# Kernel optimization log

Hardware: AMD Instinct MI355X
Metric: run time of the kernel (lower is better)

The kernel has to match this reference:

```python
import jax, jax.numpy as jnp
import numpy as np

WS = 8          # window size -> N = 64
SHIFT = 4       # shift size for shifted windows
FEAT = 32       # feature map H = W at stage 3
C = 512         # channels (SwinV2-B stage 3)
HEADS = 16
B_IMG = 128     # images -> 128 * (32/8)^2 = 2048 windows


def _rel_coords_table():
    # log-spaced continuous relative coords table, SwinV2 style: [(2W-1)^2, 2]
    r = np.arange(-(WS - 1), WS, dtype=np.float32)
    t = np.stack(np.meshgrid(r, r, indexing='ij'), axis=-1)  # [15,15,2]
    t = t / (WS - 1) * 8.0
    t = np.sign(t) * np.log2(np.abs(t) + 1.0) / np.log2(8.0)
    return t.reshape(-1, 2)


def _rel_pos_index():
    c = np.stack(np.meshgrid(np.arange(WS), np.arange(WS), indexing='ij'))  # [2,8,8]
    cf = c.reshape(2, -1)
    rel = (cf[:, :, None] - cf[:, None, :]).transpose(1, 2, 0)  # [64,64,2]
    rel[:, :, 0] += WS - 1
    rel[:, :, 1] += WS - 1
    rel[:, :, 0] *= 2 * WS - 1
    return rel.sum(-1).astype(np.int32)  # [64,64]


def _shift_mask():
    # standard SwinV2 shifted-window attention mask: [nW, N, N] in {0, -100}
    img = np.zeros((FEAT, FEAT), dtype=np.float32)
    cnt = 0
    for hs in (slice(0, -WS), slice(-WS, -SHIFT), slice(-SHIFT, None)):
        for ws in (slice(0, -WS), slice(-WS, -SHIFT), slice(-SHIFT, None)):
            img[hs, ws] = cnt
            cnt += 1
    win = img.reshape(FEAT // WS, WS, FEAT // WS, WS).transpose(0, 2, 1, 3)
    win = win.reshape(-1, WS * WS)  # [nW, 64]
    diff = win[:, None, :] - win[:, :, None]
    return np.where(diff != 0, -100.0, 0.0).astype(np.float32)


def setup_inputs() -> dict:
    key = jax.random.key(0)
    ks = jax.random.split(key, 10)
    nW = (FEAT // WS) ** 2  # 16 windows per image
    Bw = B_IMG * nW         # 2048
    N = WS * WS
    s = 0.02
    return {
        'x': jax.random.normal(ks[0], (Bw, N, C), jnp.float32),
        'mask': jnp.asarray(_shift_mask()),
        'qkv_w': jax.random.normal(ks[1], (3 * C, C), jnp.float32) * s,
        'q_bias': jnp.zeros((C,), jnp.float32),
        'v_bias': jnp.zeros((C,), jnp.float32),
        'logit_scale': jnp.full((HEADS, 1, 1), np.log(10.0), jnp.float32),
        'cpb_w1': jax.random.normal(ks[2], (512, 2), jnp.float32) * s,
        'cpb_b1': jnp.zeros((512,), jnp.float32),
        'cpb_w2': jax.random.normal(ks[3], (HEADS, 512), jnp.float32) * s,
        'proj_w': jax.random.normal(ks[4], (C, C), jnp.float32) * s,
        'proj_b': jnp.zeros((C,), jnp.float32),
        'rel_coords_table': jnp.asarray(_rel_coords_table()),
        'rel_pos_index': jnp.asarray(_rel_pos_index()),
    }


def reference(x, mask, qkv_w, q_bias, v_bias, logit_scale, cpb_w1, cpb_b1,
              cpb_w2, proj_w, proj_b, rel_coords_table, rel_pos_index):
    Bw, N, Cdim = x.shape
    H = logit_scale.shape[0]
    d = Cdim // H
    # qkv projection; k has no bias (SwinV2)
    qkv_bias = jnp.concatenate([q_bias, jnp.zeros_like(q_bias), v_bias])
    qkv = (x @ qkv_w.T + qkv_bias).reshape(Bw, N, 3, H, d).transpose(2, 0, 3, 1, 4)
    q, k, v = qkv[0], qkv[1], qkv[2]  # each [Bw,H,N,d]
    # cosine attention with learned per-head temperature
    qn = q / jnp.maximum(jnp.linalg.norm(q, axis=-1, keepdims=True), 1e-12)
    kn = k / jnp.maximum(jnp.linalg.norm(k, axis=-1, keepdims=True), 1e-12)
    attn = jnp.einsum('bhnd,bhmd->bhnm', qn, kn)
    scale = jnp.exp(jnp.minimum(logit_scale, jnp.log(100.0)))  # [H,1,1]
    attn = attn * scale[None]
    # continuous relative position bias via small MLP over log-spaced coords
    tbl = jax.nn.relu(rel_coords_table @ cpb_w1.T + cpb_b1) @ cpb_w2.T  # [(2W-1)^2,H]
    bias = tbl[rel_pos_index.reshape(-1)].reshape(N, N, H).transpose(2, 0, 1)
    attn = attn + 16.0 * jax.nn.sigmoid(bias)[None]
    # shifted-window mask applied per window group
    nW = mask.shape[0]
    attn = attn.reshape(Bw // nW, nW, H, N, N) + mask[None, :, None]
    attn = jax.nn.softmax(attn.reshape(Bw, H, N, N), axis=-1)
    out = jnp.einsum('bhnm,bhmd->bhnd', attn, v)
    out = out.transpose(0, 2, 1, 3).reshape(Bw, N, Cdim)
    return out @ proj_w.T + proj_b
```

## Files before the change

kernel.cpp:

```cpp
#include <hip/hip_runtime.h>
#include <stdint.h>
#include <stddef.h>


typedef __attribute__((ext_vector_type(8))) short bf16x8;
typedef __attribute__((ext_vector_type(4))) float f32x4;
typedef __attribute__((ext_vector_type(4))) unsigned short us4;
typedef __attribute__((ext_vector_type(8))) unsigned short us8;
typedef unsigned short u16;
typedef unsigned int u32;

#define FENCE() asm volatile("" ::: "memory")
#define WAITV4() asm volatile("s_waitcnt vmcnt(4)" ::: "memory")
#define WAITV3() asm volatile("s_waitcnt vmcnt(3)" ::: "memory")
#define WAITV0() asm volatile("s_waitcnt vmcnt(0)" ::: "memory")
#define WAITL0() asm volatile("s_waitcnt lgkmcnt(0)" ::: "memory")

__device__ __forceinline__ u16 f2bf(float f) {
  union { __bf16 b; u16 u; } cv;
  cv.b = (__bf16)f;
  return cv.u;
}
__device__ __forceinline__ float bf2f(u16 s) {
  return __uint_as_float(((u32)s) << 16);
}
__device__ __forceinline__ void gl_lds16(const void* g, void* l) {
  __builtin_amdgcn_global_load_lds(
      (const __attribute__((address_space(1))) u32*)g,
      (__attribute__((address_space(3))) u32*)l, 16, 0, 0);
}
__device__ __forceinline__ f32x4 mfma16(bf16x8 a, bf16x8 b, f32x4 c) {
  return __builtin_amdgcn_mfma_f32_16x16x32_bf16(a, b, c, 0, 0, 0);
}
__device__ __forceinline__ bf16x8 ldswz(const u16* p, int ks) {
  return *(const bf16x8*)((const u16*)((uintptr_t)p ^ (uintptr_t)(ks << 6)));
}


__global__ void conv_w_kernel(const float* __restrict__ QW, const float* __restrict__ PW,
                              u16* __restrict__ WQB, u16* __restrict__ WPB) {
  int idx = blockIdx.x * 256 + threadIdx.x;
  const int NQ = 1536 * 512 / 4;
  float4 v; u16* dst;
  if (idx < NQ) { v = ((const float4*)QW)[idx]; dst = WQB + (size_t)idx * 4; }
  else { int k = idx - NQ; v = ((const float4*)PW)[k]; dst = WPB + (size_t)k * 4; }
  us4 u; u.x = f2bf(v.x); u.y = f2bf(v.y); u.z = f2bf(v.z); u.w = f2bf(v.w);
  *(us4*)dst = u;
}

__global__ void xconv_kernel(const float* __restrict__ X, u16* __restrict__ XB) {
  size_t idx = (size_t)blockIdx.x * 256 + threadIdx.x;
  float4 a = ((const float4*)X)[idx * 2];
  float4 b = ((const float4*)X)[idx * 2 + 1];
  us8 o;
  o[0] = f2bf(a.x); o[1] = f2bf(a.y); o[2] = f2bf(a.z); o[3] = f2bf(a.w);
  o[4] = f2bf(b.x); o[5] = f2bf(b.y); o[6] = f2bf(b.z); o[7] = f2bf(b.w);
  *(us8*)&XB[idx * 8] = o;
}

__global__ void sig16_kernel(const float* __restrict__ CT, const float* __restrict__ W1,
                             const float* __restrict__ B1, const float* __restrict__ W2,
                             float* __restrict__ SIG) {
  int i = blockIdx.x;
  int tid = threadIdx.x;
  float c0 = CT[i * 2 + 0], c1 = CT[i * 2 + 1];
  float a[16];
  #pragma unroll
  for (int hh = 0; hh < 16; ++hh) a[hh] = 0.f;
  #pragma unroll
  for (int jj = 0; jj < 2; ++jj) {
    int j = tid + jj * 256;
    float h = fmaxf(c0 * W1[j * 2 + 0] + c1 * W1[j * 2 + 1] + B1[j], 0.f);
    #pragma unroll
    for (int hh = 0; hh < 16; ++hh) a[hh] += h * W2[hh * 512 + j];
  }
  __shared__ float red[4][16];
  #pragma unroll
  for (int hh = 0; hh < 16; ++hh) {
    float v = a[hh];
    for (int m = 1; m < 64; m <<= 1) v += __shfl_xor(v, m);
    if ((tid & 63) == 0) red[tid >> 6][hh] = v;
  }
  __syncthreads();
  if (tid < 16) {
    float v = red[0][tid] + red[1][tid] + red[2][tid] + red[3][tid];
    SIG[i * 16 + tid] = 16.f / (1.f + __expf(-v));
  }
}

__global__ void cmb_kernel(const float* __restrict__ SIG, const float* __restrict__ MASK,
                           const int* __restrict__ RPI, float* __restrict__ CMB) {
  int b = blockIdx.x;
  int w = b >> 4, h = b & 15;
  int tid = threadIdx.x;
  const float* mrow = &MASK[(size_t)w * 4096];
  float* crow = &CMB[(size_t)b * 4096];
  #pragma unroll
  for (int it = 0; it < 16; ++it) {
    int nm = it * 256 + tid;
    crow[nm] = SIG[RPI[nm] * 16 + h] + mrow[nm];
  }
}


#define GEMM32_KLOOP()                                                     \
  _Pragma("unroll")                                                        \
  for (int t = 0; t < 16; ++t) {                                           \
    const int Sb = (t % 3) * 12288;                                        \
    _Pragma("unroll")                                                      \
    for (int m = 0; m < 4; ++m)                                            \
      af[m] = *(const bf16x8*)&S[Sb + (wm * 64 + m * 16 + fr) * 32 + fsw]; \
    _Pragma("unroll")                                                      \
    for (int n = 0; n < 2; ++n)                                            \
      bf[n] = *(const bf16x8*)&S[Sb + 4096 + (wn * 64 + n * 16 + fr) * 32 + fsw]; \
    if (t + 2 <= 15) stageB(t + 2);                                        \
    FENCE(); __builtin_amdgcn_s_barrier(); FENCE();                        \
    WAITL0(); __builtin_amdgcn_sched_barrier(0);                           \
    __builtin_amdgcn_s_setprio(1);                                         \
    _Pragma("unroll")                                                      \
    for (int m = 0; m < 4; ++m)                                            \
      _Pragma("unroll")                                                    \
      for (int n = 0; n < 2; ++n)                                          \
        acc[m][n] = mfma16(af[m], bf[n], acc[m][n]);                       \
    __builtin_amdgcn_s_setprio(0);                                         \
    FENCE(); __builtin_amdgcn_s_barrier(); FENCE();                        \
    _Pragma("unroll")                                                      \
    for (int n = 0; n < 2; ++n)                                            \
      bf[n] = *(const bf16x8*)&S[Sb + 4096 + (wn * 64 + (n + 2) * 16 + fr) * 32 + fsw]; \
    if (t + 3 <= 15) stageA(t + 3);                                        \
    if (t <= 12) { WAITV4(); }                                             \
    else if (t == 13) { WAITV3(); }                                        \
    else if (t == 14) { WAITV0(); }                                        \
    FENCE(); __builtin_amdgcn_s_barrier(); FENCE();                        \
    WAITL0(); __builtin_amdgcn_sched_barrier(0);                           \
    __builtin_amdgcn_s_setprio(1);                                         \
    _Pragma("unroll")                                                      \
    for (int m = 0; m < 4; ++m)                                            \
      _Pragma("unroll")                                                    \
      for (int n = 0; n < 2; ++n)                                          \
        acc[m][n + 2] = mfma16(af[m], bf[n], acc[m][n + 2]);               \
    __builtin_amdgcn_s_setprio(0);                                         \
    FENCE(); __builtin_amdgcn_s_barrier(); FENCE();                        \
  }


__global__ __launch_bounds__(512, 4) void qkv_g32(
    const u16* __restrict__ XB, const u16* __restrict__ WB,
    const float* __restrict__ QB, const float* __restrict__ VB,
    u16* __restrict__ QKV) {
  __shared__ u16 S[36864];
  const int tid = threadIdx.x, lane = tid & 63, w = tid >> 6;
  int bid = blockIdx.x;
  int swz = (bid & 7) * 768 + (bid >> 3);
  const int mt = swz / 6, nt = swz - mt * 6;
  const long m0 = (long)mt * 128, n0 = (long)nt * 256;
  const int wm = w >> 2, wn = w & 3;
  const int fr = lane & 15, lg = lane >> 4;
  const int fsw = (lg ^ ((fr >> 1) & 3)) << 3;
  const f32x4 zf = {0.f, 0.f, 0.f, 0.f};

  f32x4 acc[4][4];
  #pragma unroll
  for (int mi = 0; mi < 4; ++mi)
    #pragma unroll
    for (int ni = 0; ni < 4; ++ni) acc[mi][ni] = zf;

  const int arow = tid >> 2;
  const int asc = (tid & 3) ^ ((arow >> 1) & 3);
  const u16* aSrc = &XB[(size_t)(m0 + arow) * 512 + asc * 8];
  const u16* bSrc0 = &WB[(size_t)(n0 + arow) * 512 + asc * 8];
  const u16* bSrc1 = &WB[(size_t)(n0 + 128 + arow) * 512 + asc * 8];

  auto stageA = [&](int kt) {
    gl_lds16(aSrc + kt * 32, &S[(kt % 3) * 12288 + w * 512]);
  };
  auto stageB = [&](int kt) {
    gl_lds16(bSrc0 + kt * 32, &S[(kt % 3) * 12288 + 4096 + w * 512]);
    gl_lds16(bSrc1 + kt * 32, &S[(kt % 3) * 12288 + 8192 + w * 512]);
  };

  bf16x8 af[4], bf[2];

  stageA(0); stageB(0); stageA(1); stageB(1); stageA(2);
  WAITV4();
  FENCE(); __builtin_amdgcn_s_barrier(); FENCE();

  GEMM32_KLOOP()

  u16* eb = &S[w * 4608];
  #pragma unroll
  for (int ni = 0; ni < 4; ++ni) {
    const long c = n0 + wn * 64 + ni * 16 + fr;
    float bias = (c < 512) ? QB[c] : (c < 1024 ? 0.f : VB[c - 1024]);
    #pragma unroll
    for (int mi = 0; mi < 4; ++mi)
      #pragma unroll
      for (int r = 0; r < 4; ++r)
        eb[(mi * 16 + lg * 4 + r) * 72 + ni * 16 + fr] = f2bf(acc[mi][ni][r] + bias);
  }
  WAITL0();
  #pragma unroll
  for (int i = 0; i < 8; ++i) {
    int row = i * 8 + (lane >> 3);
    int c16 = lane & 7;
    us8 v = *(const us8*)&eb[row * 72 + c16 * 8];
    *(us8*)&QKV[(size_t)(m0 + wm * 64 + row) * 1536 + n0 + wn * 64 + c16 * 8] = v;
  }
}


__global__ __launch_bounds__(512, 4) void proj_g32(
    const u16* __restrict__ A, const u16* __restrict__ WB,
    const float* __restrict__ PB, float* __restrict__ OUT) {
  __shared__ u16 S[36864];
  const int tid = threadIdx.x, lane = tid & 63, w = tid >> 6;
  int bid = blockIdx.x;
  int swz = (bid & 7) * 256 + (bid >> 3);
  const int mt = swz >> 1, nt = swz & 1;
  const long m0 = (long)mt * 128, n0 = (long)nt * 256;
  const int wm = w >> 2, wn = w & 3;
  const int fr = lane & 15, lg = lane >> 4;
  const int fsw = (lg ^ ((fr >> 1) & 3)) << 3;
  const f32x4 zf = {0.f, 0.f, 0.f, 0.f};

  f32x4 acc[4][4];
  #pragma unroll
  for (int mi = 0; mi < 4; ++mi)
    #pragma unroll
    for (int ni = 0; ni < 4; ++ni) acc[mi][ni] = zf;

  const int arow = tid >> 2;
  const int asc = (tid & 3) ^ ((arow >> 1) & 3);
  const u16* aSrc = &A[(size_t)(m0 + arow) * 1536 + asc * 8];
  const u16* bSrc0 = &WB[(size_t)(n0 + arow) * 512 + asc * 8];
  const u16* bSrc1 = &WB[(size_t)(n0 + 128 + arow) * 512 + asc * 8];

  auto stageA = [&](int kt) {
    gl_lds16(aSrc + kt * 32, &S[(kt % 3) * 12288 + w * 512]);
  };
  auto stageB = [&](int kt) {
    gl_lds16(bSrc0 + kt * 32, &S[(kt % 3) * 12288 + 4096 + w * 512]);
    gl_lds16(bSrc1 + kt * 32, &S[(kt % 3) * 12288 + 8192 + w * 512]);
  };

  bf16x8 af[4], bf[2];

  stageA(0); stageB(0); stageA(1); stageB(1); stageA(2);
  WAITV4();
  FENCE(); __builtin_amdgcn_s_barrier(); FENCE();

  GEMM32_KLOOP()

  #pragma unroll
  for (int ni = 0; ni < 4; ++ni) {
    const long c = n0 + wn * 64 + ni * 16 + fr;
    float bias = PB[c];
    #pragma unroll
    for (int mi = 0; mi < 4; ++mi)
      #pragma unroll
      for (int r = 0; r < 4; ++r) {
        long row = m0 + wm * 64 + mi * 16 + lg * 4 + r;
        OUT[row * 512 + c] = acc[mi][ni][r] + bias;
      }
  }
}


__global__ __launch_bounds__(256, 2) void qkv_gemm_rs(
    const float* __restrict__ X, const u16* __restrict__ WB,
    const float* __restrict__ QB, const float* __restrict__ VB,
    u16* __restrict__ QKV) {
  __shared__ u16 As[128 * 64];
  __shared__ u16 Bs[128 * 64];
  const int tid = threadIdx.x, lane = tid & 63, w = tid >> 6;
  int bid = blockIdx.x;
  int swz = (bid & 7) * 1536 + (bid >> 3);
  const int mt = swz / 12, nt = swz - mt * 12;
  const long m0 = (long)mt * 128, n0 = (long)nt * 128;
  const int wm = w >> 1, wn = w & 1;
  const f32x4 zf = {0.f, 0.f, 0.f, 0.f};

  f32x4 acc[4][4];
  #pragma unroll
  for (int mi = 0; mi < 4; ++mi)
    #pragma unroll
    for (int ni = 0; ni < 4; ++ni) acc[mi][ni] = zf;

  const int fr = lane & 15;
  const int fsw = ((lane >> 4) ^ (lane & 7)) * 8;
  const u16* Ap = &As[(wm * 64 + fr) * 64 + fsw];
  const u16* Bp = &Bs[(wn * 64 + fr) * 64 + fsw];

  for (int t = 0; t < 8; ++t) {
    float4 av[8];
    #pragma unroll
    for (int i = 0; i < 8; ++i) {
      int ch = tid + (i << 8);
      int row = ch >> 4, kc = ch & 15;
      av[i] = *(const float4*)&X[(m0 + row) * 512 + t * 64 + kc * 4];
    }
    #pragma unroll
    for (int i = 0; i < 4; ++i) {
      int ch = ((w << 2) + i) * 64 + lane;
      int row = ch >> 3, kc = (ch & 7) ^ (row & 7);
      gl_lds16(&WB[(n0 + row) * 512 + t * 64 + kc * 8], &Bs[((w << 2) + i) * 512]);
    }
    #pragma unroll
    for (int i = 0; i < 8; ++i) {
      int ch = tid + (i << 8);
      int row = ch >> 4, kc = ch & 15;
      int kcs = kc ^ ((row & 7) << 1);
      us4 u; u.x = f2bf(av[i].x); u.y = f2bf(av[i].y); u.z = f2bf(av[i].z); u.w = f2bf(av[i].w);
      *(us4*)&As[row * 64 + kcs * 4] = u;
    }
    __syncthreads();
    #pragma unroll
    for (int ks = 0; ks < 2; ++ks) {
      bf16x8 af[4], bfr[4];
      #pragma unroll
      for (int mi = 0; mi < 4; ++mi) af[mi] = ldswz(Ap + mi * 1024, ks);
      #pragma unroll
      for (int ni = 0; ni < 4; ++ni) bfr[ni] = ldswz(Bp + ni * 1024, ks);
      #pragma unroll
      for (int mi = 0; mi < 4; ++mi)
        #pragma unroll
        for (int ni = 0; ni < 4; ++ni)
          acc[mi][ni] = mfma16(af[mi], bfr[ni], acc[mi][ni]);
    }
    __syncthreads();
  }

  #pragma unroll
  for (int ni = 0; ni < 4; ++ni) {
    const long c = n0 + wn * 64 + ni * 16 + (lane & 15);
    float bias = (c < 512) ? QB[c] : (c < 1024 ? 0.f : VB[c - 1024]);
    #pragma unroll
    for (int mi = 0; mi < 4; ++mi)
      #pragma unroll
      for (int r = 0; r < 4; ++r) {
        long row = m0 + wm * 64 + mi * 16 + (lane >> 4) * 4 + r;
        QKV[row * 1536 + c] = f2bf(acc[mi][ni][r] + bias);
      }
  }
}


__global__ __launch_bounds__(256, 3) void attn_wh(
    u16* __restrict__ QKV, const float* __restrict__ CMB, const float* __restrict__ LS) {
  __shared__ u16 smu[26112];
  const int tid = threadIdx.x, lane = tid & 63, w = tid >> 6;
  const int b = blockIdx.x;
  const int win = b >> 2;
  const int h = (b & 3) * 4 + w;
  const int wi = win & 15;
  const size_t base = (size_t)win * 64 * 1536;
  const int fr = lane & 15, lg = lane >> 4;
  u16* ps = &smu[w * 6528];
  u16* vt = ps + 4352;
  const float scale = __expf(fminf(LS[h], 4.6051702f));
  const float* cp = &CMB[((size_t)(wi * 16 + h)) << 12];
  const f32x4 zf = {0.f, 0.f, 0.f, 0.f};

  us8 vrow[4];
  #pragma unroll
  for (int c = 0; c < 4; ++c)
    vrow[c] = *(const us8*)&QKV[base + (size_t)lane * 1536 + 1024 + h * 32 + c * 8];

  f32x4 acc[4][4];
  #pragma unroll
  for (int m = 0; m < 4; ++m)
    #pragma unroll
    for (int n = 0; n < 4; ++n)
      #pragma unroll
      for (int r = 0; r < 4; ++r)
        acc[m][n][r] = cp[(m * 16 + lg * 4 + r) * 64 + n * 16 + fr];

  bf16x8 af[4], bk[4];
  #pragma unroll
  for (int m = 0; m < 4; ++m) {
    us8 qv = *(const us8*)&QKV[base + (size_t)(m * 16 + fr) * 1536 + h * 32 + lg * 8];
    float qf[8]; float ss = 0.f;
    #pragma unroll
    for (int j = 0; j < 8; ++j) { qf[j] = bf2f(qv[j]); ss += qf[j] * qf[j]; }
    ss += __shfl_xor(ss, 16); ss += __shfl_xor(ss, 32);
    float rn = scale / fmaxf(sqrtf(ss), 1e-12f);
    union { us8 u; bf16x8 b; } cv;
    #pragma unroll
    for (int j = 0; j < 8; ++j) cv.u[j] = f2bf(qf[j] * rn);
    af[m] = cv.b;
  }
  #pragma unroll
  for (int m = 0; m < 4; ++m) {
    us8 kv = *(const us8*)&QKV[base + (size_t)(m * 16 + fr) * 1536 + 512 + h * 32 + lg * 8];
    float kf[8]; float ss = 0.f;
    #pragma unroll
    for (int j = 0; j < 8; ++j) { kf[j] = bf2f(kv[j]); ss += kf[j] * kf[j]; }
    ss += __shfl_xor(ss, 16); ss += __shfl_xor(ss, 32);
    float rn = 1.f / fmaxf(sqrtf(ss), 1e-12f);
    union { us8 u; bf16x8 b; } cv;
    #pragma unroll
    for (int j = 0; j < 8; ++j) cv.u[j] = f2bf(kf[j] * rn);
    bk[m] = cv.b;
  }

  #pragma unroll
  for (int m = 0; m < 4; ++m)
    #pragma unroll
    for (int n = 0; n < 4; ++n)
      acc[m][n] = mfma16(af[m], bk[n], acc[m][n]);

  #pragma unroll
  for (int c = 0; c < 4; ++c)
    #pragma unroll
    for (int j = 0; j < 8; ++j)
      vt[(c * 8 + j) * 68 + lane] = vrow[c][j];

  #pragma unroll
  for (int m = 0; m < 4; ++m)
    #pragma unroll
    for (int r = 0; r < 4; ++r) {
      float pv[4];
      float mx = -3.0e38f;
      #pragma unroll
      for (int n = 0; n < 4; ++n) { pv[n] = acc[m][n][r]; mx = fmaxf(mx, pv[n]); }
      mx = fmaxf(mx, __shfl_xor(mx, 1));
      mx = fmaxf(mx, __shfl_xor(mx, 2));
      mx = fmaxf(mx, __shfl_xor(mx, 4));
      mx = fmaxf(mx, __shfl_xor(mx, 8));
      float sum = 0.f;
      #pragma unroll
      for (int n = 0; n < 4; ++n) { pv[n] = __expf(pv[n] - mx); sum += pv[n]; }
      sum += __shfl_xor(sum, 1); sum += __shfl_xor(sum, 2);
      sum += __shfl_xor(sum, 4); sum += __shfl_xor(sum, 8);
      float inv = 1.f / sum;
      #pragma unroll
      for (int n = 0; n < 4; ++n)
        ps[(m * 16 + lg * 4 + r) * 68 + n * 16 + fr] = f2bf(pv[n] * inv);
    }

  WAITL0(); __builtin_amdgcn_sched_barrier(0);

  f32x4 o[4][2];
  #pragma unroll
  for (int m = 0; m < 4; ++m) { o[m][0] = zf; o[m][1] = zf; }
  #pragma unroll
  for (int m = 0; m < 4; ++m)
    #pragma unroll
    for (int ks = 0; ks < 2; ++ks) {
      bf16x8 ap = *(const bf16x8*)&ps[(m * 16 + fr) * 68 + ks * 32 + lg * 8];
      #pragma unroll
      for (int n2 = 0; n2 < 2; ++n2) {
        bf16x8 bv = *(const bf16x8*)&vt[(n2 * 16 + fr) * 68 + ks * 32 + lg * 8];
        o[m][n2] = mfma16(ap, bv, o[m][n2]);
      }
    }

  #pragma unroll
  for (int m = 0; m < 4; ++m)
    #pragma unroll
    for (int n2 = 0; n2 < 2; ++n2)
      #pragma unroll
      for (int r = 0; r < 4; ++r)
        QKV[base + (size_t)(m * 16 + lg * 4 + r) * 1536 + h * 32 + n2 * 16 + fr] =
            f2bf(o[m][n2][r]);
}


extern "C" void kernel_launch(void* const* d_in, const int* in_sizes, int n_in,
                              void* d_out, int out_size, void* d_ws, size_t ws_size,
                              hipStream_t stream) {
  const float* X    = (const float*)d_in[0];
  const float* MASK = (const float*)d_in[1];
  const float* QW   = (const float*)d_in[2];
  const float* QB   = (const float*)d_in[3];
  const float* VB   = (const float*)d_in[4];
  const float* LS   = (const float*)d_in[5];
  const float* CW1  = (const float*)d_in[6];
  const float* CB1  = (const float*)d_in[7];
  const float* CW2  = (const float*)d_in[8];
  const float* PW   = (const float*)d_in[9];
  const float* PB   = (const float*)d_in[10];
  const float* CT   = (const float*)d_in[11];
  const int*   RPI  = (const int*)d_in[12];
  float* OUT = (float*)d_out;

  char* ws = (char*)d_ws;
  const bool big = ws_size >= 543178752ull;
  u16* QKV = (u16*)ws;
  u16* XB  = (u16*)(ws + 402653184ull);
  size_t off = big ? 536870912ull : 402653184ull;
  float* CMB = (float*)(ws + off);  off += 4194304ull;
  float* SIG = (float*)(ws + off);  off += 16384ull;
  u16*   WQB = (u16*)(ws + off);    off += 1572864ull;
  u16*   WPB = (u16*)(ws + off);

  conv_w_kernel<<<1024, 256, 0, stream>>>(QW, PW, WQB, WPB);
  sig16_kernel<<<225, 256, 0, stream>>>(CT, CW1, CB1, CW2, SIG);
  cmb_kernel<<<256, 256, 0, stream>>>(SIG, MASK, RPI, CMB);
  if (big) {
    xconv_kernel<<<32768, 256, 0, stream>>>(X, XB);
    qkv_g32<<<6144, 512, 0, stream>>>(XB, WQB, QB, VB, QKV);
  } else {
    qkv_gemm_rs<<<12288, 256, 0, stream>>>(X, WQB, QB, VB, QKV);
  }
  attn_wh<<<8192, 256, 0, stream>>>(QKV, CMB, LS);
  proj_g32<<<2048, 512, 0, stream>>>(QKV, WPB, PB, OUT);
}
```

Before: 641.7 us.

## Store QKV in per-window per-head contiguous layout and stage attention output via LDS

The QKV intermediate buffer changes from row-major [token, 1536] to a [window, q/k/v, head, 64 tokens, 32 dims] layout. Each head's Q/K/V tile becomes a contiguous 4 KB block, so the attention kernel's loads are fully coalesced instead of 64-byte strided rows. The QKV GEMM epilogues, the attention output write (now staged through LDS and stored as 16-byte vectors) and the projection GEMM's A-operand addressing are all updated to match. The risk is that the projection GEMM now reads A from scattered 64-byte pieces per k-tile, and the LDS staging adds a wait in the attention kernel.

```diff
diff --git a/kernel.cpp b/kernel.cpp
--- a/kernel.cpp
+++ b/kernel.cpp
@@ -199,12 +199,15 @@
         eb[(mi * 16 + lg * 4 + r) * 72 + ni * 16 + fr] = f2bf(acc[mi][ni][r] + bias);
   }
   WAITL0();
+  const int c16 = lane & 7;
+  const int colc = (int)n0 + wn * 64 + c16 * 8;
+  const size_t whoff = (size_t)(colc >> 9) * 32768 + (size_t)((colc >> 5) & 15) * 2048 + (colc & 31);
   #pragma unroll
   for (int i = 0; i < 8; ++i) {
-    int row = i * 8 + (lane >> 3);
-    int c16 = lane & 7;
-    us8 v = *(const us8*)&eb[row * 72 + c16 * 8];
-    *(us8*)&QKV[(size_t)(m0 + wm * 64 + row) * 1536 + n0 + wn * 64 + c16 * 8] = v;
+    int rowl = i * 8 + (lane >> 3);
+    long row = m0 + wm * 64 + rowl;
+    us8 v = *(const us8*)&eb[rowl * 72 + c16 * 8];
+    *(us8*)&QKV[(size_t)(row >> 6) * 98304 + whoff + (row & 63) * 32] = v;
   }
 }
 
@@ -231,12 +234,12 @@
 
   const int arow = tid >> 2;
   const int asc = (tid & 3) ^ ((arow >> 1) & 3);
-  const u16* aSrc = &A[(size_t)(m0 + arow) * 1536 + asc * 8];
+  const u16* aSrc = &A[(size_t)((m0 >> 6) + (arow >> 6)) * 98304 + (size_t)(arow & 63) * 32 + asc * 8];
   const u16* bSrc0 = &WB[(size_t)(n0 + arow) * 512 + asc * 8];
   const u16* bSrc1 = &WB[(size_t)(n0 + 128 + arow) * 512 + asc * 8];
 
   auto stageA = [&](int kt) {
-    gl_lds16(aSrc + kt * 32, &S[(kt % 3) * 12288 + w * 512]);
+    gl_lds16(aSrc + kt * 2048, &S[(kt % 3) * 12288 + w * 512]);
   };
   auto stageB = [&](int kt) {
     gl_lds16(bSrc0 + kt * 32, &S[(kt % 3) * 12288 + 4096 + w * 512]);
@@ -334,12 +337,13 @@
   for (int ni = 0; ni < 4; ++ni) {
     const long c = n0 + wn * 64 + ni * 16 + (lane & 15);
     float bias = (c < 512) ? QB[c] : (c < 1024 ? 0.f : VB[c - 1024]);
+    const size_t whoff = (size_t)(c >> 9) * 32768 + (size_t)((c >> 5) & 15) * 2048 + (c & 31);
     #pragma unroll
     for (int mi = 0; mi < 4; ++mi)
       #pragma unroll
       for (int r = 0; r < 4; ++r) {
         long row = m0 + wm * 64 + mi * 16 + (lane >> 4) * 4 + r;
-        QKV[row * 1536 + c] = f2bf(acc[mi][ni][r] + bias);
+        QKV[(size_t)(row >> 6) * 98304 + whoff + (row & 63) * 32] = f2bf(acc[mi][ni][r] + bias);
       }
   }
 }
@@ -353,10 +357,12 @@
   const int win = b >> 2;
   const int h = (b & 3) * 4 + w;
   const int wi = win & 15;
-  const size_t base = (size_t)win * 64 * 1536;
   const int fr = lane & 15, lg = lane >> 4;
   u16* ps = &smu[w * 6528];
   u16* vt = ps + 4352;
+  const u16* Qb = &QKV[(size_t)win * 98304 + (size_t)h * 2048];
+  const u16* Kb = Qb + 32768;
+  const u16* Vb = Qb + 65536;
   const float scale = __expf(fminf(LS[h], 4.6051702f));
   const float* cp = &CMB[((size_t)(wi * 16 + h)) << 12];
   const f32x4 zf = {0.f, 0.f, 0.f, 0.f};
@@ -364,7 +370,7 @@
   us8 vrow[4];
   #pragma unroll
   for (int c = 0; c < 4; ++c)
-    vrow[c] = *(const us8*)&QKV[base + (size_t)lane * 1536 + 1024 + h * 32 + c * 8];
+    vrow[c] = *(const us8*)&Vb[lane * 32 + c * 8];
 
   f32x4 acc[4][4];
   #pragma unroll
@@ -378,7 +384,7 @@
   bf16x8 af[4], bk[4];
   #pragma unroll
   for (int m = 0; m < 4; ++m) {
-    us8 qv = *(const us8*)&QKV[base + (size_t)(m * 16 + fr) * 1536 + h * 32 + lg * 8];
+    us8 qv = *(const us8*)&Qb[(m * 16 + fr) * 32 + lg * 8];
     float qf[8]; float ss = 0.f;
     #pragma unroll
     for (int j = 0; j < 8; ++j) { qf[j] = bf2f(qv[j]); ss += qf[j] * qf[j]; }
@@ -391,7 +397,7 @@
   }
   #pragma unroll
   for (int m = 0; m < 4; ++m) {
-    us8 kv = *(const us8*)&QKV[base + (size_t)(m * 16 + fr) * 1536 + 512 + h * 32 + lg * 8];
+    us8 kv = *(const us8*)&Kb[(m * 16 + fr) * 32 + lg * 8];
     float kf[8]; float ss = 0.f;
     #pragma unroll
     for (int j = 0; j < 8; ++j) { kf[j] = bf2f(kv[j]); ss += kf[j] * kf[j]; }
@@ -461,8 +467,12 @@
     for (int n2 = 0; n2 < 2; ++n2)
       #pragma unroll
       for (int r = 0; r < 4; ++r)
-        QKV[base + (size_t)(m * 16 + lg * 4 + r) * 1536 + h * 32 + n2 * 16 + fr] =
-            f2bf(o[m][n2][r]);
+        ps[(m * 16 + lg * 4 + r) * 68 + n2 * 16 + fr] = f2bf(o[m][n2][r]);
+  WAITL0(); __builtin_amdgcn_sched_barrier(0);
+  u16* dstO = (u16*)&QKV[(size_t)win * 98304 + (size_t)h * 2048 + lane * 32];
+  #pragma unroll
+  for (int c = 0; c < 4; ++c)
+    *(us8*)&dstO[c * 8] = *(const us8*)&ps[lane * 68 + c * 8];
 }
 
 
```

New measurement: 647.4 us. No clear change (+0.9%).

## Fuse fp32-to-bf16 input conversion into the pipelined QKV GEMM

Applied to the files above, without the earlier changes.

The separate xconv pass and the fallback register-staged GEMM are removed. The pipelined qkv_g32 kernel now loads fp32 X tiles into registers two steps ahead, converts them to bf16 and writes them swizzled into LDS, while B tiles keep using direct global-to-LDS loads. This drops a full read and write of a 128 MB bf16 copy of the activations and the workspace-size branch. In exchange the A stream reads twice the bytes per tile through registers, which raises register pressure and changes the wait-count pipelining.

```diff
diff --git a/kernel.cpp b/kernel.cpp
--- a/kernel.cpp
+++ b/kernel.cpp
@@ -31,9 +31,6 @@
 }
 __device__ __forceinline__ f32x4 mfma16(bf16x8 a, bf16x8 b, f32x4 c) {
   return __builtin_amdgcn_mfma_f32_16x16x32_bf16(a, b, c, 0, 0, 0);
-}
-__device__ __forceinline__ bf16x8 ldswz(const u16* p, int ks) {
-  return *(const bf16x8*)((const u16*)((uintptr_t)p ^ (uintptr_t)(ks << 6)));
 }
 
 
@@ -48,16 +45,6 @@
   *(us4*)dst = u;
 }
 
-__global__ void xconv_kernel(const float* __restrict__ X, u16* __restrict__ XB) {
-  size_t idx = (size_t)blockIdx.x * 256 + threadIdx.x;
-  float4 a = ((const float4*)X)[idx * 2];
-  float4 b = ((const float4*)X)[idx * 2 + 1];
-  us8 o;
-  o[0] = f2bf(a.x); o[1] = f2bf(a.y); o[2] = f2bf(a.z); o[3] = f2bf(a.w);
-  o[4] = f2bf(b.x); o[5] = f2bf(b.y); o[6] = f2bf(b.z); o[7] = f2bf(b.w);
-  *(us8*)&XB[idx * 8] = o;
-}
-
 __global__ void sig16_kernel(const float* __restrict__ CT, const float* __restrict__ W1,
                              const float* __restrict__ B1, const float* __restrict__ W2,
                              float* __restrict__ SIG) {
@@ -103,49 +90,8 @@
 }
 
 
-#define GEMM32_KLOOP()                                                     \
-  _Pragma("unroll")                                                        \
-  for (int t = 0; t < 16; ++t) {                                           \
-    const int Sb = (t % 3) * 12288;                                        \
-    _Pragma("unroll")                                                      \
-    for (int m = 0; m < 4; ++m)                                            \
-      af[m] = *(const bf16x8*)&S[Sb + (wm * 64 + m * 16 + fr) * 32 + fsw]; \
-    _Pragma("unroll")                                                      \
-    for (int n = 0; n < 2; ++n)                                            \
-      bf[n] = *(const bf16x8*)&S[Sb + 4096 + (wn * 64 + n * 16 + fr) * 32 + fsw]; \
-    if (t + 2 <= 15) stageB(t + 2);                                        \
-    FENCE(); __builtin_amdgcn_s_barrier(); FENCE();                        \
-    WAITL0(); __builtin_amdgcn_sched_barrier(0);                           \
-    __builtin_amdgcn_s_setprio(1);                                         \
-    _Pragma("unroll")                                                      \
-    for (int m = 0; m < 4; ++m)                                            \
-      _Pragma("unroll")                                                    \
-      for (int n = 0; n < 2; ++n)                                          \
-        acc[m][n] = mfma16(af[m], bf[n], acc[m][n]);                       \
-    __builtin_amdgcn_s_setprio(0);                                         \
-    FENCE(); __builtin_amdgcn_s_barrier(); FENCE();                        \
-    _Pragma("unroll")                                                      \
-    for (int n = 0; n < 2; ++n)                                            \
-      bf[n] = *(const bf16x8*)&S[Sb + 4096 + (wn * 64 + (n + 2) * 16 + fr) * 32 + fsw]; \
-    if (t + 3 <= 15) stageA(t + 3);                                        \
-    if (t <= 12) { WAITV4(); }                                             \
-    else if (t == 13) { WAITV3(); }                                        \
-    else if (t == 14) { WAITV0(); }                                        \
-    FENCE(); __builtin_amdgcn_s_barrier(); FENCE();                        \
-    WAITL0(); __builtin_amdgcn_sched_barrier(0);                           \
-    __builtin_amdgcn_s_setprio(1);                                         \
-    _Pragma("unroll")                                                      \
-    for (int m = 0; m < 4; ++m)                                            \
-      _Pragma("unroll")                                                    \
-      for (int n = 0; n < 2; ++n)                                          \
-        acc[m][n + 2] = mfma16(af[m], bf[n], acc[m][n + 2]);               \
-    __builtin_amdgcn_s_setprio(0);                                         \
-    FENCE(); __builtin_amdgcn_s_barrier(); FENCE();                        \
-  }
-
-
 __global__ __launch_bounds__(512, 4) void qkv_g32(
-    const u16* __restrict__ XB, const u16* __restrict__ WB,
+    const float* __restrict__ X, const u16* __restrict__ WB,
     const float* __restrict__ QB, const float* __restrict__ VB,
     u16* __restrict__ QKV) {
   __shared__ u16 S[36864];
@@ -166,13 +112,24 @@
     for (int ni = 0; ni < 4; ++ni) acc[mi][ni] = zf;
 
   const int arow = tid >> 2;
-  const int asc = (tid & 3) ^ ((arow >> 1) & 3);
-  const u16* aSrc = &XB[(size_t)(m0 + arow) * 512 + asc * 8];
-  const u16* bSrc0 = &WB[(size_t)(n0 + arow) * 512 + asc * 8];
-  const u16* bSrc1 = &WB[(size_t)(n0 + 128 + arow) * 512 + asc * 8];
-
-  auto stageA = [&](int kt) {
-    gl_lds16(aSrc + kt * 32, &S[(kt % 3) * 12288 + w * 512]);
+  const int asc = tid & 3;
+  const int achk = asc ^ ((arow >> 1) & 3);
+  const int bsc = (tid & 3) ^ ((arow >> 1) & 3);
+  const float* aSrc = &X[(size_t)(m0 + arow) * 512 + asc * 8];
+  const u16* bSrc0 = &WB[(size_t)(n0 + arow) * 512 + bsc * 8];
+  const u16* bSrc1 = &WB[(size_t)(n0 + 128 + arow) * 512 + bsc * 8];
+
+  auto loadA = [&](int kt, float4* dst) {
+    dst[0] = *(const float4*)(aSrc + kt * 32);
+    dst[1] = *(const float4*)(aSrc + kt * 32 + 4);
+  };
+  auto writeA = [&](int kt, const float4* src) {
+    us8 o;
+    o[0] = f2bf(src[0].x); o[1] = f2bf(src[0].y);
+    o[2] = f2bf(src[0].z); o[3] = f2bf(src[0].w);
+    o[4] = f2bf(src[1].x); o[5] = f2bf(src[1].y);
+    o[6] = f2bf(src[1].z); o[7] = f2bf(src[1].w);
+    *(us8*)&S[(kt % 3) * 12288 + arow * 32 + achk * 8] = o;
   };
   auto stageB = [&](int kt) {
     gl_lds16(bSrc0 + kt * 32, &S[(kt % 3) * 12288 + 4096 + w * 512]);
@@ -180,12 +137,53 @@
   };
 
   bf16x8 af[4], bf[2];
-
-  stageA(0); stageB(0); stageA(1); stageB(1); stageA(2);
+  float4 av0[2], av1[2];
+
+  loadA(0, av0); stageB(0);
+  loadA(1, av1); stageB(1);
   WAITV4();
+  writeA(0, av0);
+  WAITL0();
   FENCE(); __builtin_amdgcn_s_barrier(); FENCE();
 
-  GEMM32_KLOOP()
+  #pragma unroll
+  for (int t = 0; t < 16; ++t) {
+    const int Sb = (t % 3) * 12288;
+    #pragma unroll
+    for (int m = 0; m < 4; ++m)
+      af[m] = *(const bf16x8*)&S[Sb + (wm * 64 + m * 16 + fr) * 32 + fsw];
+    #pragma unroll
+    for (int n = 0; n < 2; ++n)
+      bf[n] = *(const bf16x8*)&S[Sb + 4096 + (wn * 64 + n * 16 + fr) * 32 + fsw];
+    if (t + 2 <= 15) { loadA(t + 2, (t & 1) ? av1 : av0); stageB(t + 2); }
+    FENCE(); __builtin_amdgcn_s_barrier(); FENCE();
+    WAITL0(); __builtin_amdgcn_sched_barrier(0);
+    __builtin_amdgcn_s_setprio(1);
+    #pragma unroll
+    for (int m = 0; m < 4; ++m)
+      #pragma unroll
+      for (int n = 0; n < 2; ++n)
+        acc[m][n] = mfma16(af[m], bf[n], acc[m][n]);
+    __builtin_amdgcn_s_setprio(0);
+    FENCE(); __builtin_amdgcn_s_barrier(); FENCE();
+    #pragma unroll
+    for (int n = 0; n < 2; ++n)
+      bf[n] = *(const bf16x8*)&S[Sb + 4096 + (wn * 64 + (n + 2) * 16 + fr) * 32 + fsw];
+    if (t + 1 <= 15) {
+      if (t + 2 <= 15) { WAITV4(); } else { WAITV0(); }
+      writeA(t + 1, ((t + 1) & 1) ? av1 : av0);
+    }
+    FENCE(); __builtin_amdgcn_s_barrier(); FENCE();
+    WAITL0(); __builtin_amdgcn_sched_barrier(0);
+    __builtin_amdgcn_s_setprio(1);
+    #pragma unroll
+    for (int m = 0; m < 4; ++m)
+      #pragma unroll
+      for (int n = 0; n < 2; ++n)
+        acc[m][n + 2] = mfma16(af[m], bf[n], acc[m][n + 2]);
+    __builtin_amdgcn_s_setprio(0);
+    FENCE(); __builtin_amdgcn_s_barrier(); FENCE();
+  }
 
   u16* eb = &S[w * 4608];
   #pragma unroll
@@ -249,7 +247,44 @@
   WAITV4();
   FENCE(); __builtin_amdgcn_s_barrier(); FENCE();
 
-  GEMM32_KLOOP()
+  #pragma unroll
+  for (int t = 0; t < 16; ++t) {
+    const int Sb = (t % 3) * 12288;
+    #pragma unroll
+    for (int m = 0; m < 4; ++m)
+      af[m] = *(const bf16x8*)&S[Sb + (wm * 64 + m * 16 + fr) * 32 + fsw];
+    #pragma unroll
+    for (int n = 0; n < 2; ++n)
+      bf[n] = *(const bf16x8*)&S[Sb + 4096 + (wn * 64 + n * 16 + fr) * 32 + fsw];
+    if (t + 2 <= 15) stageB(t + 2);
+    FENCE(); __builtin_amdgcn_s_barrier(); FENCE();
+    WAITL0(); __builtin_amdgcn_sched_barrier(0);
+    __builtin_amdgcn_s_setprio(1);
+    #pragma unroll
+    for (int m = 0; m < 4; ++m)
+      #pragma unroll
+      for (int n = 0; n < 2; ++n)
+        acc[m][n] = mfma16(af[m], bf[n], acc[m][n]);
+    __builtin_amdgcn_s_setprio(0);
+    FENCE(); __builtin_amdgcn_s_barrier(); FENCE();
+    #pragma unroll
+    for (int n = 0; n < 2; ++n)
+      bf[n] = *(const bf16x8*)&S[Sb + 4096 + (wn * 64 + (n + 2) * 16 + fr) * 32 + fsw];
+    if (t + 3 <= 15) stageA(t + 3);
+    if (t <= 12) { WAITV4(); }
+    else if (t == 13) { WAITV3(); }
+    else if (t == 14) { WAITV0(); }
+    FENCE(); __builtin_amdgcn_s_barrier(); FENCE();
+    WAITL0(); __builtin_amdgcn_sched_barrier(0);
+    __builtin_amdgcn_s_setprio(1);
+    #pragma unroll
+    for (int m = 0; m < 4; ++m)
+      #pragma unroll
+      for (int n = 0; n < 2; ++n)
+        acc[m][n + 2] = mfma16(af[m], bf[n], acc[m][n + 2]);
+    __builtin_amdgcn_s_setprio(0);
+    FENCE(); __builtin_amdgcn_s_barrier(); FENCE();
+  }
 
   #pragma unroll
   for (int ni = 0; ni < 4; ++ni) {
@@ -261,85 +296,6 @@
       for (int r = 0; r < 4; ++r) {
         long row = m0 + wm * 64 + mi * 16 + lg * 4 + r;
         OUT[row * 512 + c] = acc[mi][ni][r] + bias;
-      }
-  }
-}
-
-
-__global__ __launch_bounds__(256, 2) void qkv_gemm_rs(
-    const float* __restrict__ X, const u16* __restrict__ WB,
-    const float* __restrict__ QB, const float* __restrict__ VB,
-    u16* __restrict__ QKV) {
-  __shared__ u16 As[128 * 64];
-  __shared__ u16 Bs[128 * 64];
-  const int tid = threadIdx.x, lane = tid & 63, w = tid >> 6;
-  int bid = blockIdx.x;
-  int swz = (bid & 7) * 1536 + (bid >> 3);
-  const int mt = swz / 12, nt = swz - mt * 12;
-  const long m0 = (long)mt * 128, n0 = (long)nt * 128;
-  const int wm = w >> 1, wn = w & 1;
-  const f32x4 zf = {0.f, 0.f, 0.f, 0.f};
-
-  f32x4 acc[4][4];
-  #pragma unroll
-  for (int mi = 0; mi < 4; ++mi)
-    #pragma unroll
-    for (int ni = 0; ni < 4; ++ni) acc[mi][ni] = zf;
-
-  const int fr = lane & 15;
-  const int fsw = ((lane >> 4) ^ (lane & 7)) * 8;
-  const u16* Ap = &As[(wm * 64 + fr) * 64 + fsw];
-  const u16* Bp = &Bs[(wn * 64 + fr) * 64 + fsw];
-
-  for (int t = 0; t < 8; ++t) {
-    float4 av[8];
-    #pragma unroll
-    for (int i = 0; i < 8; ++i) {
-      int ch = tid + (i << 8);
-      int row = ch >> 4, kc = ch & 15;
-      av[i] = *(const float4*)&X[(m0 + row) * 512 + t * 64 + kc * 4];
-    }
-    #pragma unroll
-    for (int i = 0; i < 4; ++i) {
-      int ch = ((w << 2) + i) * 64 + lane;
-      int row = ch >> 3, kc = (ch & 7) ^ (row & 7);
-      gl_lds16(&WB[(n0 + row) * 512 + t * 64 + kc * 8], &Bs[((w << 2) + i) * 512]);
-    }
-    #pragma unroll
-    for (int i = 0; i < 8; ++i) {
-      int ch = tid + (i << 8);
-      int row = ch >> 4, kc = ch & 15;
-      int kcs = kc ^ ((row & 7) << 1);
-      us4 u; u.x = f2bf(av[i].x); u.y = f2bf(av[i].y); u.z = f2bf(av[i].z); u.w = f2bf(av[i].w);
-      *(us4*)&As[row * 64 + kcs * 4] = u;
-    }
-    __syncthreads();
-    #pragma unroll
-    for (int ks = 0; ks < 2; ++ks) {
-      bf16x8 af[4], bfr[4];
-      #pragma unroll
-      for (int mi = 0; mi < 4; ++mi) af[mi] = ldswz(Ap + mi * 1024, ks);
-      #pragma unroll
-      for (int ni = 0; ni < 4; ++ni) bfr[ni] = ldswz(Bp + ni * 1024, ks);
-      #pragma unroll
-      for (int mi = 0; mi < 4; ++mi)
-        #pragma unroll
-        for (int ni = 0; ni < 4; ++ni)
-          acc[mi][ni] = mfma16(af[mi], bfr[ni], acc[mi][ni]);
-    }
-    __syncthreads();
-  }
-
-  #pragma unroll
-  for (int ni = 0; ni < 4; ++ni) {
-    const long c = n0 + wn * 64 + ni * 16 + (lane & 15);
-    float bias = (c < 512) ? QB[c] : (c < 1024 ? 0.f : VB[c - 1024]);
-    #pragma unroll
-    for (int mi = 0; mi < 4; ++mi)
-      #pragma unroll
-      for (int r = 0; r < 4; ++r) {
-        long row = m0 + wm * 64 + mi * 16 + (lane >> 4) * 4 + r;
-        QKV[row * 1536 + c] = f2bf(acc[mi][ni][r] + bias);
       }
   }
 }
@@ -485,24 +441,16 @@
   float* OUT = (float*)d_out;
 
   char* ws = (char*)d_ws;
-  const bool big = ws_size >= 543178752ull;
-  u16* QKV = (u16*)ws;
-  u16* XB  = (u16*)(ws + 402653184ull);
-  size_t off = big ? 536870912ull : 402653184ull;
-  float* CMB = (float*)(ws + off);  off += 4194304ull;
-  float* SIG = (float*)(ws + off);  off += 16384ull;
-  u16*   WQB = (u16*)(ws + off);    off += 1572864ull;
-  u16*   WPB = (u16*)(ws + off);
+  u16*   QKV = (u16*)ws;
+  float* CMB = (float*)(ws + 402653184ull);
+  float* SIG = (float*)(ws + 406847488ull);
+  u16*   WQB = (u16*)(ws + 406863872ull);
+  u16*   WPB = (u16*)(ws + 408436736ull);
 
   conv_w_kernel<<<1024, 256, 0, stream>>>(QW, PW, WQB, WPB);
   sig16_kernel<<<225, 256, 0, stream>>>(CT, CW1, CB1, CW2, SIG);
   cmb_kernel<<<256, 256, 0, stream>>>(SIG, MASK, RPI, CMB);
-  if (big) {
-    xconv_kernel<<<32768, 256, 0, stream>>>(X, XB);
-    qkv_g32<<<6144, 512, 0, stream>>>(XB, WQB, QB, VB, QKV);
-  } else {
-    qkv_gemm_rs<<<12288, 256, 0, stream>>>(X, WQB, QB, VB, QKV);
-  }
+  qkv_g32<<<6144, 512, 0, stream>>>(X, WQB, QB, VB, QKV);
   attn_wh<<<8192, 256, 0, stream>>>(QKV, CMB, LS);
   proj_g32<<<2048, 512, 0, stream>>>(QKV, WPB, PB, OUT);
 }
```

Result: slower. 673.0 us (+4.9%).
